# Kernel tuning notes

Measured on AMD Instinct MI355X. Metric: run time of the kernel, lower is better.

Reference implementation:

```python
import jax, jax.numpy as jnp
import numpy as np

B, D, K, L, H = 16384, 1024, 512, 128, 64  # batch, input_dim, num_components, latent_dim, phi hidden
EPS = 1e-9


def setup_inputs() -> dict:
    key = jax.random.key(0)
    k0, k1, k2, k3 = jax.random.split(key, 4)
    # small scales keep squared distances O(1-10) so exp(-d2) is non-degenerate
    x = jax.random.normal(k0, (B, D), jnp.float32) * 0.03
    z_samples = jax.random.normal(k1, (K, L), jnp.float32)
    W1 = jax.random.normal(k2, (L, H), jnp.float32) * (1.0 / np.sqrt(L)).astype(np.float32)
    b1 = jnp.zeros((H,), jnp.float32)
    W2 = jax.random.normal(k3, (H, D), jnp.float32) * 0.01
    b2 = jnp.zeros((D,), jnp.float32)
    return {"x": x, "z_samples": z_samples, "W1": W1, "b1": b1, "W2": W2, "b2": b2}


def reference(x, z_samples, W1, b1, W2, b2):
    # PhiNet: Linear -> ReLU -> Linear, applied to all components at once
    phi = jnp.maximum(z_samples @ W1 + b1, 0.0) @ W2 + b2          # (K, D)
    # ||x - phi_k||^2 for all (k, b) via GEMM expansion (fuses the per-component loop)
    sq = (jnp.sum(phi * phi, axis=-1)[:, None]
          + jnp.sum(x * x, axis=-1)[None, :]
          - 2.0 * (phi @ x.T))                                      # (K, B)
    lik = jnp.exp(-sq)                                              # (K, B)
    # weights = 1/K; sum_k w * lik = mean over K
    mixture_ll = jnp.log(jnp.mean(lik, axis=0) + EPS)               # (B,)
    return mixture_ll.mean()
```

## Files before the change

kernel.cpp:

```cpp
#include <hip/hip_runtime.h>
#include <hip/hip_bf16.h>
#include <stdint.h>

#define N_B   16384
#define D_DIM 1024
#define K_K   512
#define L_DIM 128
#define H_DIM 64

typedef __attribute__((ext_vector_type(8))) short short8;
typedef __attribute__((ext_vector_type(4))) float f32x4;

__device__ __forceinline__ unsigned short f2bf(float f) {
    union { float f; unsigned int u; } c; c.f = f;
    unsigned int u = c.u;
    unsigned int r = (u + 0x7FFFu + ((u >> 16) & 1u)) >> 16;
    return (unsigned short)r;
}

__device__ __forceinline__ unsigned int pk2(float a, float b) {
    __hip_bfloat162 t = __float22bfloat162_rn(make_float2(a, b));
    union { __hip_bfloat162 h; unsigned int u; } c; c.h = t;
    return c.u;
}

__global__ __launch_bounds__(256) void prep_kernel(
    const float* __restrict__ z, const float* __restrict__ W1,
    const float* __restrict__ b1, const float* __restrict__ W2,
    const float* __restrict__ b2, unsigned short* __restrict__ W2bf,
    unsigned short* __restrict__ h_bf, float* __restrict__ phi2) {
    __shared__ float zsh[8][L_DIM];
    __shared__ float hsh[8][H_DIM];
    __shared__ float redp[4][8];
    const int tid = threadIdx.x;
    const int k0 = blockIdx.x * 8;

    {
        int i = blockIdx.x * 256 + tid;
        float4 v = ((const float4*)W2)[i];
        uint2 o = make_uint2(pk2(v.x, v.y), pk2(v.z, v.w));
        *(uint2*)(W2bf + i * 4) = o;
    }
#pragma unroll
    for (int c = 0; c < 4; ++c) {
        int idx = c * 256 + tid;
        zsh[idx >> 7][idx & 127] = z[k0 * L_DIM + idx];
    }
    __syncthreads();
    {
        const int j = tid & 63, kk = tid >> 6;
        float bb = b1[j];
        float s0 = bb, s1 = bb;
        for (int l = 0; l < L_DIM; ++l) {
            float w = W1[l * H_DIM + j];
            s0 += zsh[kk][l] * w;
            s1 += zsh[kk + 4][l] * w;
        }
        float h0 = fmaxf(s0, 0.0f), h1 = fmaxf(s1, 0.0f);
        hsh[kk][j] = h0; hsh[kk + 4][j] = h1;
        h_bf[(k0 + kk) * H_DIM + j]     = f2bf(h0);
        h_bf[(k0 + kk + 4) * H_DIM + j] = f2bf(h1);
    }
    __syncthreads();
    float ss[8] = {0.f, 0.f, 0.f, 0.f, 0.f, 0.f, 0.f, 0.f};
#pragma unroll
    for (int c = 0; c < 4; ++c) {
        int d = c * 256 + tid;
        float bb = b2[d];
        float a[8];
#pragma unroll
        for (int kk = 0; kk < 8; ++kk) a[kk] = bb;
        for (int j = 0; j < H_DIM; ++j) {
            float w = W2[j * D_DIM + d];
#pragma unroll
            for (int kk = 0; kk < 8; ++kk) a[kk] += hsh[kk][j] * w;
        }
#pragma unroll
        for (int kk = 0; kk < 8; ++kk) ss[kk] += a[kk] * a[kk];
    }
    const int lane = tid & 63, wv = tid >> 6;
#pragma unroll
    for (int kk = 0; kk < 8; ++kk) {
        float v = ss[kk];
#pragma unroll
        for (int o = 1; o < 64; o <<= 1) v += __shfl_xor(v, o, 64);
        if (lane == 0) redp[wv][kk] = v;
    }
    __syncthreads();
    if (tid < 8) phi2[k0 + tid] = redp[0][tid] + redp[1][tid] + redp[2][tid] + redp[3][tid];
}

__global__ __launch_bounds__(256) void main_kernel(
    const float* __restrict__ x, const unsigned short* __restrict__ W2bf,
    const unsigned short* __restrict__ h_bf, const float* __restrict__ phi2,
    const float* __restrict__ b2, float* __restrict__ out) {
    __shared__ float upart[4][32][68];
    __shared__ __align__(16) unsigned short u_tile[32 * 72];
    __shared__ float phi2s[K_K];
    __shared__ __align__(16) float b2l[D_DIM];
    __shared__ float x2s[32], xb2s[32];
    __shared__ float red[4][32];

    const int tid = threadIdx.x;
    const int wv  = tid >> 6;
    const int l   = tid & 63;
    const int lm  = l & 15;
    const int q   = l >> 4;
    const int n0  = blockIdx.x * 32;

    phi2s[tid]       = phi2[tid];
    phi2s[256 + tid] = phi2[256 + tid];
    ((float4*)b2l)[tid] = ((const float4*)b2)[tid];
    if (tid < 32) { x2s[tid] = 0.f; xb2s[tid] = 0.f; }
    __syncthreads();

    f32x4 c1[2][4] = {};
    float x2p0 = 0.f, x2p1 = 0.f, xbp0 = 0.f, xbp1 = 0.f;
    const int dq = wv * 256;
#pragma unroll
    for (int s = 0; s < 8; ++s) {
        const int dl = dq + s * 32 + q * 8;
        float4 bb0 = *(const float4*)&b2l[dl];
        float4 bb1 = *(const float4*)&b2l[dl + 4];
        short8 af[2];
#pragma unroll
        for (int i = 0; i < 2; ++i) {
            const float* xp = x + (size_t)(n0 + i * 16 + lm) * D_DIM + dl;
            float4 v0 = *(const float4*)xp;
            float4 v1 = *(const float4*)(xp + 4);
            float s2 = v0.x*v0.x + v0.y*v0.y + v0.z*v0.z + v0.w*v0.w
                     + v1.x*v1.x + v1.y*v1.y + v1.z*v1.z + v1.w*v1.w;
            float sb = v0.x*bb0.x + v0.y*bb0.y + v0.z*bb0.z + v0.w*bb0.w
                     + v1.x*bb1.x + v1.y*bb1.y + v1.z*bb1.z + v1.w*bb1.w;
            union { short8 s8; unsigned int u[4]; } packu;
            packu.u[0] = pk2(v0.x, v0.y);
            packu.u[1] = pk2(v0.z, v0.w);
            packu.u[2] = pk2(v1.x, v1.y);
            packu.u[3] = pk2(v1.z, v1.w);
            af[i] = packu.s8;
            if (i == 0) { x2p0 += s2; xbp0 += sb; } else { x2p1 += s2; xbp1 += sb; }
        }
        short8 bfr[4];
#pragma unroll
        for (int j = 0; j < 4; ++j)
            bfr[j] = *(const short8*)(W2bf + (size_t)(j * 16 + lm) * D_DIM + dl);
#pragma unroll
        for (int i = 0; i < 2; ++i)
#pragma unroll
            for (int j = 0; j < 4; ++j)
                c1[i][j] = __builtin_amdgcn_mfma_f32_16x16x32_bf16(af[i], bfr[j], c1[i][j], 0, 0, 0);
    }
#pragma unroll
    for (int i = 0; i < 2; ++i)
#pragma unroll
        for (int j = 0; j < 4; ++j)
#pragma unroll
            for (int r = 0; r < 4; ++r)
                upart[wv][i * 16 + q * 4 + r][j * 16 + lm] = c1[i][j][r];
    {
        float v0 = x2p0, v1 = x2p1, w0 = xbp0, w1 = xbp1;
        v0 += __shfl_xor(v0, 16, 64); v0 += __shfl_xor(v0, 32, 64);
        v1 += __shfl_xor(v1, 16, 64); v1 += __shfl_xor(v1, 32, 64);
        w0 += __shfl_xor(w0, 16, 64); w0 += __shfl_xor(w0, 32, 64);
        w1 += __shfl_xor(w1, 16, 64); w1 += __shfl_xor(w1, 32, 64);
        if (l < 16) {
            atomicAdd(&x2s[l], v0);       atomicAdd(&x2s[16 + l], v1);
            atomicAdd(&xb2s[l], w0);      atomicAdd(&xb2s[16 + l], w1);
        }
    }
    __syncthreads();
#pragma unroll
    for (int c = 0; c < 8; ++c) {
        int idx = c * 256 + tid;
        int row = idx >> 6, col = idx & 63;
        float sum = upart[0][row][col] + upart[1][row][col]
                  + upart[2][row][col] + upart[3][row][col];
        u_tile[row * 72 + col] = f2bf(sum);
    }
    __syncthreads();

    f32x4 acc[8][2] = {};
#pragma unroll
    for (int ks = 0; ks < 2; ++ks) {
        const int ko = ks * 32 + q * 8;
        short8 bfr[2];
#pragma unroll
        for (int j = 0; j < 2; ++j)
            bfr[j] = *(const short8*)&u_tile[(j * 16 + lm) * 72 + ko];
#pragma unroll
        for (int i = 0; i < 8; ++i) {
            short8 a = *(const short8*)(h_bf + (size_t)(wv * 128 + i * 16 + lm) * H_DIM + ko);
#pragma unroll
            for (int j = 0; j < 2; ++j)
                acc[i][j] = __builtin_amdgcn_mfma_f32_16x16x32_bf16(a, bfr[j], acc[i][j], 0, 0, 0);
        }
    }
    float xn0 = x2s[lm]      - 2.f * xb2s[lm];
    float xn1 = x2s[16 + lm] - 2.f * xb2s[16 + lm];
    float cs0 = 0.f, cs1 = 0.f;
#pragma unroll
    for (int i = 0; i < 8; ++i) {
#pragma unroll
        for (int r = 0; r < 4; ++r) {
            float p2 = phi2s[wv * 128 + i * 16 + q * 4 + r];
            cs0 += __expf(-(p2 + xn0 - 2.f * acc[i][0][r]));
            cs1 += __expf(-(p2 + xn1 - 2.f * acc[i][1][r]));
        }
    }
    cs0 += __shfl_xor(cs0, 16, 64); cs0 += __shfl_xor(cs0, 32, 64);
    cs1 += __shfl_xor(cs1, 16, 64); cs1 += __shfl_xor(cs1, 32, 64);
    if (l < 16) { red[wv][l] = cs0; red[wv][16 + l] = cs1; }
    __syncthreads();
    if (tid < 32) {
        float row_lik = red[0][tid] + red[1][tid] + red[2][tid] + red[3][tid];
        float lg = __logf(row_lik * (1.0f / (float)K_K) + 1e-9f);
        lg += __shfl_xor(lg, 1, 64);
        lg += __shfl_xor(lg, 2, 64);
        lg += __shfl_xor(lg, 4, 64);
        lg += __shfl_xor(lg, 8, 64);
        lg += __shfl_xor(lg, 16, 64);
        if (tid == 0) atomicAdd(out, lg * (1.0f / (float)N_B));
    }
}

extern "C" void kernel_launch(void* const* d_in, const int* in_sizes, int n_in,
                              void* d_out, int out_size, void* d_ws, size_t ws_size,
                              hipStream_t stream) {
    const float* x  = (const float*)d_in[0];
    const float* z  = (const float*)d_in[1];
    const float* W1 = (const float*)d_in[2];
    const float* b1 = (const float*)d_in[3];
    const float* W2 = (const float*)d_in[4];
    const float* b2 = (const float*)d_in[5];

    char* ws = (char*)d_ws;
    unsigned short* W2bf = (unsigned short*)(ws);
    unsigned short* h_bf = (unsigned short*)(ws + 131072);
    float*          phi2 = (float*)(ws + 196608);

    hipMemsetAsync(d_out, 0, sizeof(float), stream);
    prep_kernel<<<64, 256, 0, stream>>>(z, W1, b1, W2, b2, W2bf, h_bf, phi2);
    main_kernel<<<N_B / 32, 256, 0, stream>>>(x, W2bf, h_bf, phi2, b2, (float*)d_out);
}
```

Measured before the change: 149.0 us.

## Prefetch x tile into registers and double-buffer W2 fragments in main kernel

Every x value a thread needs (32 float4 per thread) is loaded at kernel start, before the shared-memory setup barrier. W2 bf16 fragments are double-buffered across the eight k-steps so each step's global loads overlap the previous step's MFMAs. The shared-memory atomicAdd reduction of row norms is replaced by per-wave partial arrays summed at read time. This raises register pressure, which may reduce occupancy.

```diff
diff --git a/kernel.cpp b/kernel.cpp
--- a/kernel.cpp
+++ b/kernel.cpp
@@ -98,7 +98,7 @@
     __shared__ __align__(16) unsigned short u_tile[32 * 72];
     __shared__ float phi2s[K_K];
     __shared__ __align__(16) float b2l[D_DIM];
-    __shared__ float x2s[32], xb2s[32];
+    __shared__ float x2p4[4][32], xb2p4[4][32];
     __shared__ float red[4][32];
 
     const int tid = threadIdx.x;
@@ -107,27 +107,45 @@
     const int lm  = l & 15;
     const int q   = l >> 4;
     const int n0  = blockIdx.x * 32;
-
+    const int dq  = wv * 256;
+
+    float4 xv[2][8][2];
+#pragma unroll
+    for (int i = 0; i < 2; ++i) {
+        const float* xp = x + (size_t)(n0 + i * 16 + lm) * D_DIM + dq + q * 8;
+#pragma unroll
+        for (int s = 0; s < 8; ++s) {
+            xv[i][s][0] = *(const float4*)(xp + s * 32);
+            xv[i][s][1] = *(const float4*)(xp + s * 32 + 4);
+        }
+    }
     phi2s[tid]       = phi2[tid];
     phi2s[256 + tid] = phi2[256 + tid];
     ((float4*)b2l)[tid] = ((const float4*)b2)[tid];
-    if (tid < 32) { x2s[tid] = 0.f; xb2s[tid] = 0.f; }
-    __syncthreads();
+    __syncthreads();
+
+    short8 wf[2][4];
+#pragma unroll
+    for (int j = 0; j < 4; ++j)
+        wf[0][j] = *(const short8*)(W2bf + (size_t)(j * 16 + lm) * D_DIM + dq + q * 8);
 
     f32x4 c1[2][4] = {};
     float x2p0 = 0.f, x2p1 = 0.f, xbp0 = 0.f, xbp1 = 0.f;
-    const int dq = wv * 256;
 #pragma unroll
     for (int s = 0; s < 8; ++s) {
+        const int cur = s & 1, nxt = cur ^ 1;
+        if (s < 7) {
+#pragma unroll
+            for (int j = 0; j < 4; ++j)
+                wf[nxt][j] = *(const short8*)(W2bf + (size_t)(j * 16 + lm) * D_DIM + dq + (s + 1) * 32 + q * 8);
+        }
         const int dl = dq + s * 32 + q * 8;
         float4 bb0 = *(const float4*)&b2l[dl];
         float4 bb1 = *(const float4*)&b2l[dl + 4];
         short8 af[2];
 #pragma unroll
         for (int i = 0; i < 2; ++i) {
-            const float* xp = x + (size_t)(n0 + i * 16 + lm) * D_DIM + dl;
-            float4 v0 = *(const float4*)xp;
-            float4 v1 = *(const float4*)(xp + 4);
+            float4 v0 = xv[i][s][0], v1 = xv[i][s][1];
             float s2 = v0.x*v0.x + v0.y*v0.y + v0.z*v0.z + v0.w*v0.w
                      + v1.x*v1.x + v1.y*v1.y + v1.z*v1.z + v1.w*v1.w;
             float sb = v0.x*bb0.x + v0.y*bb0.y + v0.z*bb0.z + v0.w*bb0.w
@@ -140,15 +158,11 @@
             af[i] = packu.s8;
             if (i == 0) { x2p0 += s2; xbp0 += sb; } else { x2p1 += s2; xbp1 += sb; }
         }
-        short8 bfr[4];
-#pragma unroll
-        for (int j = 0; j < 4; ++j)
-            bfr[j] = *(const short8*)(W2bf + (size_t)(j * 16 + lm) * D_DIM + dl);
 #pragma unroll
         for (int i = 0; i < 2; ++i)
 #pragma unroll
             for (int j = 0; j < 4; ++j)
-                c1[i][j] = __builtin_amdgcn_mfma_f32_16x16x32_bf16(af[i], bfr[j], c1[i][j], 0, 0, 0);
+                c1[i][j] = __builtin_amdgcn_mfma_f32_16x16x32_bf16(af[i], wf[cur][j], c1[i][j], 0, 0, 0);
     }
 #pragma unroll
     for (int i = 0; i < 2; ++i)
@@ -157,16 +171,13 @@
 #pragma unroll
             for (int r = 0; r < 4; ++r)
                 upart[wv][i * 16 + q * 4 + r][j * 16 + lm] = c1[i][j][r];
-    {
-        float v0 = x2p0, v1 = x2p1, w0 = xbp0, w1 = xbp1;
-        v0 += __shfl_xor(v0, 16, 64); v0 += __shfl_xor(v0, 32, 64);
-        v1 += __shfl_xor(v1, 16, 64); v1 += __shfl_xor(v1, 32, 64);
-        w0 += __shfl_xor(w0, 16, 64); w0 += __shfl_xor(w0, 32, 64);
-        w1 += __shfl_xor(w1, 16, 64); w1 += __shfl_xor(w1, 32, 64);
-        if (l < 16) {
-            atomicAdd(&x2s[l], v0);       atomicAdd(&x2s[16 + l], v1);
-            atomicAdd(&xb2s[l], w0);      atomicAdd(&xb2s[16 + l], w1);
-        }
+    x2p0 += __shfl_xor(x2p0, 16, 64); x2p0 += __shfl_xor(x2p0, 32, 64);
+    x2p1 += __shfl_xor(x2p1, 16, 64); x2p1 += __shfl_xor(x2p1, 32, 64);
+    xbp0 += __shfl_xor(xbp0, 16, 64); xbp0 += __shfl_xor(xbp0, 32, 64);
+    xbp1 += __shfl_xor(xbp1, 16, 64); xbp1 += __shfl_xor(xbp1, 32, 64);
+    if (l < 16) {
+        x2p4[wv][l] = x2p0;  x2p4[wv][16 + l] = x2p1;
+        xb2p4[wv][l] = xbp0; xb2p4[wv][16 + l] = xbp1;
     }
     __syncthreads();
 #pragma unroll
@@ -195,8 +206,10 @@
                 acc[i][j] = __builtin_amdgcn_mfma_f32_16x16x32_bf16(a, bfr[j], acc[i][j], 0, 0, 0);
         }
     }
-    float xn0 = x2s[lm]      - 2.f * xb2s[lm];
-    float xn1 = x2s[16 + lm] - 2.f * xb2s[16 + lm];
+    float xn0 = (x2p4[0][lm] + x2p4[1][lm] + x2p4[2][lm] + x2p4[3][lm])
+        - 2.f * (xb2p4[0][lm] + xb2p4[1][lm] + xb2p4[2][lm] + xb2p4[3][lm]);
+    float xn1 = (x2p4[0][16 + lm] + x2p4[1][16 + lm] + x2p4[2][16 + lm] + x2p4[3][16 + lm])
+        - 2.f * (xb2p4[0][16 + lm] + xb2p4[1][16 + lm] + xb2p4[2][16 + lm] + xb2p4[3][16 + lm]);
     float cs0 = 0.f, cs1 = 0.f;
 #pragma unroll
     for (int i = 0; i < 8; ++i) {
```

Result: no change. 150.0 us (+0.7%).

## Stage x tile as bf16 in LDS and split first GEMM by output columns

Applied to the files above, without the earlier changes.

Each block now loads its 32 rows of x with coalesced row-wise reads, computes the squared norms and bias dot products, and stores a bf16 copy in shared memory. The x·W2ᵀ GEMM is then split across waves by output columns, with each wave covering the full 1024 reduction dimension, instead of by reduction slices. This removes the four-way partial-sum buffer, its extra reduction pass and the shared-memory atomics. In exchange it uses about 66KB of LDS for the x tile, which may lower occupancy, and each wave now reads every x row from LDS.

```diff
diff --git a/kernel.cpp b/kernel.cpp
--- a/kernel.cpp
+++ b/kernel.cpp
@@ -7,6 +7,7 @@
 #define K_K   512
 #define L_DIM 128
 #define H_DIM 64
+#define SX    1032
 
 typedef __attribute__((ext_vector_type(8))) short short8;
 typedef __attribute__((ext_vector_type(4))) float f32x4;
@@ -94,10 +95,9 @@
     const float* __restrict__ x, const unsigned short* __restrict__ W2bf,
     const unsigned short* __restrict__ h_bf, const float* __restrict__ phi2,
     const float* __restrict__ b2, float* __restrict__ out) {
-    __shared__ float upart[4][32][68];
+    __shared__ __align__(16) unsigned short x_bf[32 * SX];
     __shared__ __align__(16) unsigned short u_tile[32 * 72];
     __shared__ float phi2s[K_K];
-    __shared__ __align__(16) float b2l[D_DIM];
     __shared__ float x2s[32], xb2s[32];
     __shared__ float red[4][32];
 
@@ -108,75 +108,54 @@
     const int q   = l >> 4;
     const int n0  = blockIdx.x * 32;
 
+    float4 b2r[4];
+#pragma unroll
+    for (int sub = 0; sub < 4; ++sub)
+        b2r[sub] = ((const float4*)b2)[sub * 64 + l];
+
+    float x2a[8], xba[8];
+#pragma unroll
+    for (int it = 0; it < 8; ++it) {
+        const int r = it * 4 + wv;
+        const float* xrow = x + (size_t)(n0 + r) * D_DIM;
+        float s2 = 0.f, sb = 0.f;
+#pragma unroll
+        for (int sub = 0; sub < 4; ++sub) {
+            float4 v = *(const float4*)(xrow + sub * 256 + l * 4);
+            s2 += v.x*v.x + v.y*v.y + v.z*v.z + v.w*v.w;
+            sb += v.x*b2r[sub].x + v.y*b2r[sub].y + v.z*b2r[sub].z + v.w*b2r[sub].w;
+            uint2 o = make_uint2(pk2(v.x, v.y), pk2(v.z, v.w));
+            *(uint2*)&x_bf[r * SX + sub * 256 + l * 4] = o;
+        }
+        x2a[it] = s2; xba[it] = sb;
+    }
     phi2s[tid]       = phi2[tid];
     phi2s[256 + tid] = phi2[256 + tid];
-    ((float4*)b2l)[tid] = ((const float4*)b2)[tid];
-    if (tid < 32) { x2s[tid] = 0.f; xb2s[tid] = 0.f; }
-    __syncthreads();
-
-    f32x4 c1[2][4] = {};
-    float x2p0 = 0.f, x2p1 = 0.f, xbp0 = 0.f, xbp1 = 0.f;
-    const int dq = wv * 256;
-#pragma unroll
-    for (int s = 0; s < 8; ++s) {
-        const int dl = dq + s * 32 + q * 8;
-        float4 bb0 = *(const float4*)&b2l[dl];
-        float4 bb1 = *(const float4*)&b2l[dl + 4];
-        short8 af[2];
-#pragma unroll
-        for (int i = 0; i < 2; ++i) {
-            const float* xp = x + (size_t)(n0 + i * 16 + lm) * D_DIM + dl;
-            float4 v0 = *(const float4*)xp;
-            float4 v1 = *(const float4*)(xp + 4);
-            float s2 = v0.x*v0.x + v0.y*v0.y + v0.z*v0.z + v0.w*v0.w
-                     + v1.x*v1.x + v1.y*v1.y + v1.z*v1.z + v1.w*v1.w;
-            float sb = v0.x*bb0.x + v0.y*bb0.y + v0.z*bb0.z + v0.w*bb0.w
-                     + v1.x*bb1.x + v1.y*bb1.y + v1.z*bb1.z + v1.w*bb1.w;
-            union { short8 s8; unsigned int u[4]; } packu;
-            packu.u[0] = pk2(v0.x, v0.y);
-            packu.u[1] = pk2(v0.z, v0.w);
-            packu.u[2] = pk2(v1.x, v1.y);
-            packu.u[3] = pk2(v1.z, v1.w);
-            af[i] = packu.s8;
-            if (i == 0) { x2p0 += s2; xbp0 += sb; } else { x2p1 += s2; xbp1 += sb; }
-        }
-        short8 bfr[4];
-#pragma unroll
-        for (int j = 0; j < 4; ++j)
-            bfr[j] = *(const short8*)(W2bf + (size_t)(j * 16 + lm) * D_DIM + dl);
-#pragma unroll
-        for (int i = 0; i < 2; ++i)
-#pragma unroll
-            for (int j = 0; j < 4; ++j)
-                c1[i][j] = __builtin_amdgcn_mfma_f32_16x16x32_bf16(af[i], bfr[j], c1[i][j], 0, 0, 0);
+#pragma unroll
+    for (int it = 0; it < 8; ++it) {
+        float a = x2a[it], b = xba[it];
+#pragma unroll
+        for (int o = 1; o < 64; o <<= 1) { a += __shfl_xor(a, o, 64); b += __shfl_xor(b, o, 64); }
+        if (l == 0) { x2s[it * 4 + wv] = a; xb2s[it * 4 + wv] = b; }
+    }
+    __syncthreads();
+
+    f32x4 c1[2] = {};
+    const unsigned short* w2row = W2bf + (size_t)(wv * 16 + lm) * D_DIM;
+#pragma unroll
+    for (int ks = 0; ks < 32; ++ks) {
+        const int k0 = ks * 32 + q * 8;
+        short8 bw = *(const short8*)(w2row + k0);
+        short8 a0 = *(const short8*)&x_bf[lm * SX + k0];
+        short8 a1 = *(const short8*)&x_bf[(16 + lm) * SX + k0];
+        c1[0] = __builtin_amdgcn_mfma_f32_16x16x32_bf16(a0, bw, c1[0], 0, 0, 0);
+        c1[1] = __builtin_amdgcn_mfma_f32_16x16x32_bf16(a1, bw, c1[1], 0, 0, 0);
     }
 #pragma unroll
     for (int i = 0; i < 2; ++i)
 #pragma unroll
-        for (int j = 0; j < 4; ++j)
-#pragma unroll
-            for (int r = 0; r < 4; ++r)
-                upart[wv][i * 16 + q * 4 + r][j * 16 + lm] = c1[i][j][r];
-    {
-        float v0 = x2p0, v1 = x2p1, w0 = xbp0, w1 = xbp1;
-        v0 += __shfl_xor(v0, 16, 64); v0 += __shfl_xor(v0, 32, 64);
-        v1 += __shfl_xor(v1, 16, 64); v1 += __shfl_xor(v1, 32, 64);
-        w0 += __shfl_xor(w0, 16, 64); w0 += __shfl_xor(w0, 32, 64);
-        w1 += __shfl_xor(w1, 16, 64); w1 += __shfl_xor(w1, 32, 64);
-        if (l < 16) {
-            atomicAdd(&x2s[l], v0);       atomicAdd(&x2s[16 + l], v1);
-            atomicAdd(&xb2s[l], w0);      atomicAdd(&xb2s[16 + l], w1);
-        }
-    }
-    __syncthreads();
-#pragma unroll
-    for (int c = 0; c < 8; ++c) {
-        int idx = c * 256 + tid;
-        int row = idx >> 6, col = idx & 63;
-        float sum = upart[0][row][col] + upart[1][row][col]
-                  + upart[2][row][col] + upart[3][row][col];
-        u_tile[row * 72 + col] = f2bf(sum);
-    }
+        for (int r = 0; r < 4; ++r)
+            u_tile[(i * 16 + q * 4 + r) * 72 + wv * 16 + lm] = f2bf(c1[i][r]);
     __syncthreads();
 
     f32x4 acc[8][2] = {};
```

After: 146.2 us. No clear change (-1.8%).
